# Performance work log

Hardware: AMD Instinct MI355X
Metric: run time of the kernel (lower is better)

Reference implementation:

```python
import jax, jax.numpy as jnp
import numpy as np

HM_W, WH_W, OFF_W = 1.0, 0.1, 1.0  # loss_weight dict values
EPS_SIG = 1e-4


def _neg_loss(pred, gt):
    # pred already sigmoided + clamped. Modified focal loss (CornerNet).
    pos = (gt == 1.0).astype(pred.dtype)
    neg = (gt < 1.0).astype(pred.dtype)
    part1 = (pos + (2.0 * neg - 1.0) * pred) ** 2          # alpha=2
    part2 = (neg + (2.0 * pos - 1.0) * gt) ** 4            # beta=4
    part3 = jnp.log(neg + (2.0 * pos - 1.0) * pred)
    loss = -jnp.sum(part1 * part2 * part3)
    num_pos = jnp.sum(pos)
    fallback = jnp.maximum(jnp.sum((pred > 0.3).astype(pred.dtype)), 1.0)
    denom = jnp.where(num_pos == 0.0, fallback, num_pos)
    return loss / denom


def _reg_l1(pred, mask, ind, target):
    # pred: [B,C,H,W] -> gather K per-object C-dim vectors per batch via flat HW index
    B, C, H, W = pred.shape
    K = ind.shape[1]
    feat = pred.transpose(0, 2, 3, 1).reshape(B, H * W, C)  # [B,HW,C]
    idx = jnp.broadcast_to(ind[:, :, None], (B, K, C))
    gathered = jnp.take_along_axis(feat, idx, axis=1)       # [B,K,C]
    m = jnp.broadcast_to(mask[:, :, None].astype(pred.dtype), (B, K, C))
    diff = gathered * m - target * m
    ad = jnp.abs(diff)
    sl1 = jnp.where(ad < 1.0, 0.5 * diff * diff, ad - 0.5)  # smooth_l1, sum
    return jnp.sum(sl1) / (jnp.sum(m) + 1e-4)


def setup_inputs() -> dict:
    key = jax.random.key(0)
    ks = jax.random.split(key, 8)
    B, C, H, W, K = 128, 20, 128, 128, 128
    hm_pred = jax.random.normal(ks[0], (B, C, H, W), dtype=jnp.float32)
    hm_gt = jax.random.uniform(ks[1], (B, C, H, W), dtype=jnp.float32)
    # plant some exact positives (gt == 1) like real CenterNet targets
    hm_gt = hm_gt.at[:, :, 64, 64].set(1.0)
    wh_pred = jax.random.normal(ks[2], (B, 2, H, W), dtype=jnp.float32)
    wh_gt = jax.random.uniform(ks[3], (B, K, 2), dtype=jnp.float32)
    off_pred = jax.random.normal(ks[4], (B, 2, H, W), dtype=jnp.float32)
    off_gt = jax.random.uniform(ks[5], (B, K, 2), dtype=jnp.float32)
    offset_mask = jax.random.randint(ks[6], (B, K), 0, 2, dtype=jnp.int32)
    indexes = jax.random.randint(ks[7], (B, K), 0, H * W).astype(jnp.int64)
    return {"hm_pred": hm_pred, "hm_gt": hm_gt, "wh_pred": wh_pred,
            "wh_gt": wh_gt, "off_pred": off_pred, "off_gt": off_gt,
            "offset_mask": offset_mask, "indexes": indexes}


def reference(hm_pred, hm_gt, wh_pred, wh_gt, off_pred, off_gt, offset_mask, indexes):
    hm = jnp.clip(jax.nn.sigmoid(hm_pred), EPS_SIG, 1.0 - EPS_SIG)
    hm_loss = _neg_loss(hm, hm_gt)
    wh_loss = _reg_l1(wh_pred, offset_mask, indexes, wh_gt)
    off_loss = _reg_l1(off_pred, offset_mask, indexes, off_gt)
    total = HM_W * hm_loss + WH_W * wh_loss + OFF_W * off_loss
    return (hm_loss, wh_loss, off_loss, total)
```

## Files before the change

### kernel.cpp

```cpp
#include <hip/hip_runtime.h>

#define NB_HM   2048
#define NB_REG  64
#define REG_OFF (3 * NB_HM)

typedef float f32x4 __attribute__((ext_vector_type(4)));

__device__ __forceinline__ float wave_sum(float v) {
    #pragma unroll
    for (int off = 32; off > 0; off >>= 1) v += __shfl_down(v, off, 64);
    return v;
}

__device__ __forceinline__ void block_reduce_store3(float a, float b, float c,
                                                    float* __restrict__ dst) {
    a = wave_sum(a); b = wave_sum(b); c = wave_sum(c);
    __shared__ float sa[8], sb[8], sc[8];
    int lane = threadIdx.x & 63;
    int wave = threadIdx.x >> 6;
    if (lane == 0) { sa[wave] = a; sb[wave] = b; sc[wave] = c; }
    __syncthreads();
    if (threadIdx.x == 0) {
        int nw = blockDim.x >> 6;
        float ta = 0.f, tb = 0.f, tc = 0.f;
        for (int w = 0; w < nw; ++w) { ta += sa[w]; tb += sb[w]; tc += sc[w]; }
        dst[0] = ta; dst[1] = tb; dst[2] = tc;
    }
}

__device__ __forceinline__ void hm_elem(float x, float gt, float& s_loss,
                                        unsigned& posc, unsigned& cntc) {
    bool pos = (gt == 1.0f);
    float e = __expf(-x);
    float p = __builtin_amdgcn_rcpf(1.0f + e);
    p = fminf(fmaxf(p, 1e-4f), 1.0f - 1e-4f);
    float arg = pos ? p : 1.0f - p;
    float a   = 1.0f - arg;
    float b   = pos ? 1.0f : 1.0f - gt;
    float b2  = b * b;
    float l   = __logf(arg);
    s_loss += (a * a) * (b2 * b2) * l;
    posc += (unsigned)__popcll(__ballot(pos));
    cntc += (unsigned)__popcll(__ballot(p > 0.3f));
}

__device__ __forceinline__ void gload(f32x4& d, const f32x4* a) {
    asm volatile("global_load_dwordx4 %0, %1, off" : "=v"(d) : "v"(a));
}

#define SB() __builtin_amdgcn_sched_barrier(0)
#define WAITV(n) do { asm volatile("s_waitcnt vmcnt(" #n ")" ::: "memory"); SB(); } while (0)

#define COMPV(P, G)                                    \
    do {                                               \
        hm_elem((P)[0], (G)[0], s_loss, posc, cntc);   \
        hm_elem((P)[1], (G)[1], s_loss, posc, cntc);   \
        hm_elem((P)[2], (G)[2], s_loss, posc, cntc);   \
        hm_elem((P)[3], (G)[3], s_loss, posc, cntc);   \
    } while (0)

#define PH_MID(SET, CNEXT)                                        \
    do {                                                          \
        WAITV(6);                                                 \
        COMPV(P##SET, G##SET);                                    \
        SB();                                                     \
        const f32x4* _pa = pp + (long long)(CNEXT) * NT;          \
        const f32x4* _ga = gg + (long long)(CNEXT) * NT;          \
        gload(P##SET, _pa);                                       \
        gload(G##SET, _ga);                                       \
    } while (0)

#define PH_TAIL(SET, WN)                                          \
    do { WAITV(WN); COMPV(P##SET, G##SET); SB(); } while (0)

__global__ void __launch_bounds__(256)
hm_loss_kernel(const f32x4* __restrict__ p4,
               const f32x4* __restrict__ g4,
               float* __restrict__ ws, long long N4) {
    long long tid = (long long)blockIdx.x * blockDim.x + threadIdx.x;
    long long NT  = (long long)gridDim.x * blockDim.x;

    float    s_loss = 0.f;
    unsigned posc = 0, cntc = 0;

    bool clean = (N4 == 20 * NT);

    if (clean) {
        f32x4 P0, P1, P2, P3, G0, G1, G2, G3;
        const f32x4* pp = p4 + tid;
        const f32x4* gg = g4 + tid;

        gload(P0, pp);              gload(G0, gg);
        gload(P1, pp + NT);         gload(G1, gg + NT);
        gload(P2, pp + 2 * NT);     gload(G2, gg + 2 * NT);
        gload(P3, pp + 3 * NT);     gload(G3, gg + 3 * NT);

        PH_MID(0, 4);   PH_MID(1, 5);   PH_MID(2, 6);   PH_MID(3, 7);
        PH_MID(0, 8);   PH_MID(1, 9);   PH_MID(2, 10);  PH_MID(3, 11);
        PH_MID(0, 12);  PH_MID(1, 13);  PH_MID(2, 14);  PH_MID(3, 15);
        PH_MID(0, 16);  PH_MID(1, 17);  PH_MID(2, 18);  PH_MID(3, 19);

        PH_TAIL(0, 6);  PH_TAIL(1, 4);  PH_TAIL(2, 2);  PH_TAIL(3, 0);
    } else {
        for (long long i = tid; i < N4; i += NT) {
            f32x4 xp = p4[i];
            f32x4 xg = g4[i];
            COMPV(xp, xg);
        }
    }

    int lane = threadIdx.x & 63;
    float fpos = (lane == 0) ? (float)posc : 0.f;
    float fcnt = (lane == 0) ? (float)cntc : 0.f;
    block_reduce_store3(s_loss, fpos, fcnt, &ws[3 * (size_t)blockIdx.x]);
}

__device__ __forceinline__ float smooth_l1(float d) {
    float ad = fabsf(d);
    return (ad < 1.0f) ? 0.5f * d * d : ad - 0.5f;
}

__global__ void __launch_bounds__(256)
reg_loss_kernel(const float* __restrict__ wh_pred,  const float* __restrict__ wh_gt,
                const float* __restrict__ off_pred, const float* __restrict__ off_gt,
                const int* __restrict__ mask, const int* __restrict__ ind,
                float* __restrict__ ws, int BK, int K, int HW) {
    int t = blockIdx.x * blockDim.x + threadIdx.x;
    int nt = gridDim.x * blockDim.x;
    float s_wh = 0.f, s_off = 0.f, s_m = 0.f;

    for (int i = t; i < BK; i += nt) {
        int b   = i / K;
        float m = (float)mask[i];
        int idx = ind[i];
        const float* wb = wh_pred  + (size_t)b * 2 * HW;
        const float* ob = off_pred + (size_t)b * 2 * HW;
        #pragma unroll
        for (int c = 0; c < 2; ++c) {
            float gw = wb[(size_t)c * HW + idx];
            float tw = wh_gt[(size_t)i * 2 + c];
            s_wh += smooth_l1(gw * m - tw * m);

            float go = ob[(size_t)c * HW + idx];
            float to = off_gt[(size_t)i * 2 + c];
            s_off += smooth_l1(go * m - to * m);
        }
        s_m += 2.0f * m;
    }

    block_reduce_store3(s_wh, s_off, s_m, &ws[REG_OFF + 3 * (size_t)blockIdx.x]);
}

__global__ void __launch_bounds__(1024)
reduce_finalize_kernel(const float* __restrict__ ws, float* __restrict__ out) {
    float a = 0.f, b = 0.f, c = 0.f, w = 0.f, o = 0.f, m = 0.f;
    for (int i = threadIdx.x; i < NB_HM; i += 1024) {
        a += ws[3 * i + 0];
        b += ws[3 * i + 1];
        c += ws[3 * i + 2];
    }
    if (threadIdx.x < 3 * NB_REG) {
        float v = ws[REG_OFF + threadIdx.x];
        int r = threadIdx.x % 3;
        w = (r == 0) ? v : 0.f;
        o = (r == 1) ? v : 0.f;
        m = (r == 2) ? v : 0.f;
    }

    a = wave_sum(a); b = wave_sum(b); c = wave_sum(c);
    w = wave_sum(w); o = wave_sum(o); m = wave_sum(m);

    __shared__ float s[6][16];
    int lane = threadIdx.x & 63, wv = threadIdx.x >> 6;
    if (lane == 0) {
        s[0][wv] = a; s[1][wv] = b; s[2][wv] = c;
        s[3][wv] = w; s[4][wv] = o; s[5][wv] = m;
    }
    __syncthreads();
    if (threadIdx.x == 0) {
        float t[6];
        #pragma unroll
        for (int k = 0; k < 6; ++k) {
            float acc = 0.f;
            for (int q = 0; q < 16; ++q) acc += s[k][q];
            t[k] = acc;
        }
        float loss_sum = -t[0];
        float num_pos  = t[1];
        float fallback = fmaxf(t[2], 1.0f);
        float denom    = (num_pos == 0.0f) ? fallback : num_pos;
        float hm_loss  = loss_sum / denom;
        float md       = t[5] + 1e-4f;
        float wh_loss  = t[3] / md;
        float off_loss = t[4] / md;
        out[0] = hm_loss;
        out[1] = wh_loss;
        out[2] = off_loss;
        out[3] = hm_loss + 0.1f * wh_loss + off_loss;
    }
}

extern "C" void kernel_launch(void* const* d_in, const int* in_sizes, int n_in,
                              void* d_out, int out_size, void* d_ws, size_t ws_size,
                              hipStream_t stream) {
    const float* hm_pred  = (const float*)d_in[0];
    const float* hm_gt    = (const float*)d_in[1];
    const float* wh_pred  = (const float*)d_in[2];
    const float* wh_gt    = (const float*)d_in[3];
    const float* off_pred = (const float*)d_in[4];
    const float* off_gt   = (const float*)d_in[5];
    const int*   mask     = (const int*)d_in[6];
    const int*   ind      = (const int*)d_in[7];
    float*       out      = (float*)d_out;
    float*       ws       = (float*)d_ws;

    long long N  = in_sizes[0];
    int       BK = in_sizes[6];
    const int K  = 128;
    int       B  = BK / K;
    int       HW = in_sizes[2] / (2 * B);

    hm_loss_kernel<<<NB_HM, 256, 0, stream>>>((const f32x4*)hm_pred,
                                              (const f32x4*)hm_gt, ws, N >> 2);
    reg_loss_kernel<<<NB_REG, 256, 0, stream>>>(wh_pred, wh_gt, off_pred, off_gt,
                                                mask, ind, ws, BK, K, HW);
    reduce_finalize_kernel<<<1, 1024, 0, stream>>>(ws, out);
}
```

Before: 80.44 us.

## Fuse heatmap, regression and finalize into one kernel with last-block reduction

Merges the three kernel launches into one grid where the first blocks compute the heatmap focal loss and a few extra blocks compute the gathered regression losses. An atomic counter elects the last finishing block to run the final reduction, so the separate finalize launch goes away. A memset resets the counter before each launch. The hand-scheduled inline-asm load pipeline is replaced by a plain 4-way unrolled loop, which hands load scheduling back to the compiler and may lose some memory-level overlap.

```diff
diff --git a/kernel.cpp b/kernel.cpp
--- a/kernel.cpp
+++ b/kernel.cpp
@@ -1,8 +1,10 @@
 #include <hip/hip_runtime.h>
 
 #define NB_HM   2048
-#define NB_REG  64
+#define NB_REG  8
+#define NBLK    (NB_HM + NB_REG)
 #define REG_OFF (3 * NB_HM)
+#define CTR_IDX 8192
 
 typedef float f32x4 __attribute__((ext_vector_type(4)));
 
@@ -15,15 +17,15 @@
 __device__ __forceinline__ void block_reduce_store3(float a, float b, float c,
                                                     float* __restrict__ dst) {
     a = wave_sum(a); b = wave_sum(b); c = wave_sum(c);
-    __shared__ float sa[8], sb[8], sc[8];
+    __shared__ float sa[4], sb[4], sc[4];
     int lane = threadIdx.x & 63;
     int wave = threadIdx.x >> 6;
     if (lane == 0) { sa[wave] = a; sb[wave] = b; sc[wave] = c; }
     __syncthreads();
     if (threadIdx.x == 0) {
-        int nw = blockDim.x >> 6;
         float ta = 0.f, tb = 0.f, tc = 0.f;
-        for (int w = 0; w < nw; ++w) { ta += sa[w]; tb += sb[w]; tc += sc[w]; }
+        #pragma unroll
+        for (int w = 0; w < 4; ++w) { ta += sa[w]; tb += sb[w]; tc += sc[w]; }
         dst[0] = ta; dst[1] = tb; dst[2] = tc;
     }
 }
@@ -44,13 +46,6 @@
     cntc += (unsigned)__popcll(__ballot(p > 0.3f));
 }
 
-__device__ __forceinline__ void gload(f32x4& d, const f32x4* a) {
-    asm volatile("global_load_dwordx4 %0, %1, off" : "=v"(d) : "v"(a));
-}
-
-#define SB() __builtin_amdgcn_sched_barrier(0)
-#define WAITV(n) do { asm volatile("s_waitcnt vmcnt(" #n ")" ::: "memory"); SB(); } while (0)
-
 #define COMPV(P, G)                                    \
     do {                                               \
         hm_elem((P)[0], (G)[0], s_loss, posc, cntc);   \
@@ -59,144 +54,132 @@
         hm_elem((P)[3], (G)[3], s_loss, posc, cntc);   \
     } while (0)
 
-#define PH_MID(SET, CNEXT)                                        \
-    do {                                                          \
-        WAITV(6);                                                 \
-        COMPV(P##SET, G##SET);                                    \
-        SB();                                                     \
-        const f32x4* _pa = pp + (long long)(CNEXT) * NT;          \
-        const f32x4* _ga = gg + (long long)(CNEXT) * NT;          \
-        gload(P##SET, _pa);                                       \
-        gload(G##SET, _ga);                                       \
-    } while (0)
-
-#define PH_TAIL(SET, WN)                                          \
-    do { WAITV(WN); COMPV(P##SET, G##SET); SB(); } while (0)
+__device__ __forceinline__ float smooth_l1(float d) {
+    float ad = fabsf(d);
+    return (ad < 1.0f) ? 0.5f * d * d : ad - 0.5f;
+}
 
 __global__ void __launch_bounds__(256)
-hm_loss_kernel(const f32x4* __restrict__ p4,
-               const f32x4* __restrict__ g4,
-               float* __restrict__ ws, long long N4) {
-    long long tid = (long long)blockIdx.x * blockDim.x + threadIdx.x;
-    long long NT  = (long long)gridDim.x * blockDim.x;
-
-    float    s_loss = 0.f;
-    unsigned posc = 0, cntc = 0;
-
-    bool clean = (N4 == 20 * NT);
-
-    if (clean) {
-        f32x4 P0, P1, P2, P3, G0, G1, G2, G3;
-        const f32x4* pp = p4 + tid;
-        const f32x4* gg = g4 + tid;
-
-        gload(P0, pp);              gload(G0, gg);
-        gload(P1, pp + NT);         gload(G1, gg + NT);
-        gload(P2, pp + 2 * NT);     gload(G2, gg + 2 * NT);
-        gload(P3, pp + 3 * NT);     gload(G3, gg + 3 * NT);
-
-        PH_MID(0, 4);   PH_MID(1, 5);   PH_MID(2, 6);   PH_MID(3, 7);
-        PH_MID(0, 8);   PH_MID(1, 9);   PH_MID(2, 10);  PH_MID(3, 11);
-        PH_MID(0, 12);  PH_MID(1, 13);  PH_MID(2, 14);  PH_MID(3, 15);
-        PH_MID(0, 16);  PH_MID(1, 17);  PH_MID(2, 18);  PH_MID(3, 19);
-
-        PH_TAIL(0, 6);  PH_TAIL(1, 4);  PH_TAIL(2, 2);  PH_TAIL(3, 0);
-    } else {
-        for (long long i = tid; i < N4; i += NT) {
+fused_loss_kernel(const f32x4* __restrict__ p4, const f32x4* __restrict__ g4,
+                  long long N4,
+                  const float* __restrict__ wh_pred,  const float* __restrict__ wh_gt,
+                  const float* __restrict__ off_pred, const float* __restrict__ off_gt,
+                  const int* __restrict__ mask, const int* __restrict__ ind,
+                  int BK, int K, int HW,
+                  float* __restrict__ ws, float* __restrict__ out) {
+    if (blockIdx.x < NB_HM) {
+        long long tid = (long long)blockIdx.x * 256 + threadIdx.x;
+        long long NT  = (long long)NB_HM * 256;
+
+        float    s_loss = 0.f;
+        unsigned posc = 0, cntc = 0;
+
+        long long i = tid;
+        for (; i + 3 * NT < N4; i += 4 * NT) {
+            f32x4 xp0 = p4[i];
+            f32x4 xp1 = p4[i + NT];
+            f32x4 xp2 = p4[i + 2 * NT];
+            f32x4 xp3 = p4[i + 3 * NT];
+            f32x4 xg0 = g4[i];
+            f32x4 xg1 = g4[i + NT];
+            f32x4 xg2 = g4[i + 2 * NT];
+            f32x4 xg3 = g4[i + 3 * NT];
+            COMPV(xp0, xg0);
+            COMPV(xp1, xg1);
+            COMPV(xp2, xg2);
+            COMPV(xp3, xg3);
+        }
+        for (; i < N4; i += NT) {
             f32x4 xp = p4[i];
             f32x4 xg = g4[i];
             COMPV(xp, xg);
         }
-    }
-
-    int lane = threadIdx.x & 63;
-    float fpos = (lane == 0) ? (float)posc : 0.f;
-    float fcnt = (lane == 0) ? (float)cntc : 0.f;
-    block_reduce_store3(s_loss, fpos, fcnt, &ws[3 * (size_t)blockIdx.x]);
-}
-
-__device__ __forceinline__ float smooth_l1(float d) {
-    float ad = fabsf(d);
-    return (ad < 1.0f) ? 0.5f * d * d : ad - 0.5f;
-}
-
-__global__ void __launch_bounds__(256)
-reg_loss_kernel(const float* __restrict__ wh_pred,  const float* __restrict__ wh_gt,
-                const float* __restrict__ off_pred, const float* __restrict__ off_gt,
-                const int* __restrict__ mask, const int* __restrict__ ind,
-                float* __restrict__ ws, int BK, int K, int HW) {
-    int t = blockIdx.x * blockDim.x + threadIdx.x;
-    int nt = gridDim.x * blockDim.x;
-    float s_wh = 0.f, s_off = 0.f, s_m = 0.f;
-
-    for (int i = t; i < BK; i += nt) {
-        int b   = i / K;
-        float m = (float)mask[i];
-        int idx = ind[i];
-        const float* wb = wh_pred  + (size_t)b * 2 * HW;
-        const float* ob = off_pred + (size_t)b * 2 * HW;
-        #pragma unroll
-        for (int c = 0; c < 2; ++c) {
-            float gw = wb[(size_t)c * HW + idx];
-            float tw = wh_gt[(size_t)i * 2 + c];
-            s_wh += smooth_l1(gw * m - tw * m);
-
-            float go = ob[(size_t)c * HW + idx];
-            float to = off_gt[(size_t)i * 2 + c];
-            s_off += smooth_l1(go * m - to * m);
-        }
-        s_m += 2.0f * m;
-    }
-
-    block_reduce_store3(s_wh, s_off, s_m, &ws[REG_OFF + 3 * (size_t)blockIdx.x]);
-}
-
-__global__ void __launch_bounds__(1024)
-reduce_finalize_kernel(const float* __restrict__ ws, float* __restrict__ out) {
-    float a = 0.f, b = 0.f, c = 0.f, w = 0.f, o = 0.f, m = 0.f;
-    for (int i = threadIdx.x; i < NB_HM; i += 1024) {
-        a += ws[3 * i + 0];
-        b += ws[3 * i + 1];
-        c += ws[3 * i + 2];
-    }
-    if (threadIdx.x < 3 * NB_REG) {
-        float v = ws[REG_OFF + threadIdx.x];
-        int r = threadIdx.x % 3;
-        w = (r == 0) ? v : 0.f;
-        o = (r == 1) ? v : 0.f;
-        m = (r == 2) ? v : 0.f;
-    }
-
-    a = wave_sum(a); b = wave_sum(b); c = wave_sum(c);
-    w = wave_sum(w); o = wave_sum(o); m = wave_sum(m);
-
-    __shared__ float s[6][16];
-    int lane = threadIdx.x & 63, wv = threadIdx.x >> 6;
-    if (lane == 0) {
-        s[0][wv] = a; s[1][wv] = b; s[2][wv] = c;
-        s[3][wv] = w; s[4][wv] = o; s[5][wv] = m;
+
+        int lane = threadIdx.x & 63;
+        float fpos = (lane == 0) ? (float)posc : 0.f;
+        float fcnt = (lane == 0) ? (float)cntc : 0.f;
+        block_reduce_store3(s_loss, fpos, fcnt, &ws[3 * (size_t)blockIdx.x]);
+    } else {
+        int t  = (blockIdx.x - NB_HM) * 256 + threadIdx.x;
+        int nt = NB_REG * 256;
+        float s_wh = 0.f, s_off = 0.f, s_m = 0.f;
+
+        for (int i = t; i < BK; i += nt) {
+            int b   = i / K;
+            float m = (float)mask[i];
+            int idx = ind[i];
+            const float* wb = wh_pred  + (size_t)b * 2 * HW;
+            const float* ob = off_pred + (size_t)b * 2 * HW;
+            #pragma unroll
+            for (int c = 0; c < 2; ++c) {
+                float gw = wb[(size_t)c * HW + idx];
+                float tw = wh_gt[(size_t)i * 2 + c];
+                s_wh += smooth_l1(gw * m - tw * m);
+
+                float go = ob[(size_t)c * HW + idx];
+                float to = off_gt[(size_t)i * 2 + c];
+                s_off += smooth_l1(go * m - to * m);
+            }
+            s_m += 2.0f * m;
+        }
+
+        block_reduce_store3(s_wh, s_off, s_m,
+                            &ws[REG_OFF + 3 * (size_t)(blockIdx.x - NB_HM)]);
+    }
+
+    __shared__ int s_last;
+    if (threadIdx.x == 0) {
+        __threadfence();
+        int* ctr = (int*)&ws[CTR_IDX];
+        int old = atomicAdd(ctr, 1);
+        s_last = (old == NBLK - 1) ? 1 : 0;
     }
     __syncthreads();
-    if (threadIdx.x == 0) {
-        float t[6];
-        #pragma unroll
-        for (int k = 0; k < 6; ++k) {
-            float acc = 0.f;
-            for (int q = 0; q < 16; ++q) acc += s[k][q];
-            t[k] = acc;
-        }
-        float loss_sum = -t[0];
-        float num_pos  = t[1];
-        float fallback = fmaxf(t[2], 1.0f);
-        float denom    = (num_pos == 0.0f) ? fallback : num_pos;
-        float hm_loss  = loss_sum / denom;
-        float md       = t[5] + 1e-4f;
-        float wh_loss  = t[3] / md;
-        float off_loss = t[4] / md;
-        out[0] = hm_loss;
-        out[1] = wh_loss;
-        out[2] = off_loss;
-        out[3] = hm_loss + 0.1f * wh_loss + off_loss;
+    if (s_last) {
+        __threadfence();
+        float a = 0.f, b = 0.f, c = 0.f, w = 0.f, o = 0.f, m = 0.f;
+        for (int i = threadIdx.x; i < NB_HM; i += 256) {
+            a += ws[3 * i + 0];
+            b += ws[3 * i + 1];
+            c += ws[3 * i + 2];
+        }
+        if (threadIdx.x < 3 * NB_REG) {
+            float v = ws[REG_OFF + threadIdx.x];
+            int r = threadIdx.x % 3;
+            w = (r == 0) ? v : 0.f;
+            o = (r == 1) ? v : 0.f;
+            m = (r == 2) ? v : 0.f;
+        }
+
+        a = wave_sum(a); b = wave_sum(b); c = wave_sum(c);
+        w = wave_sum(w); o = wave_sum(o); m = wave_sum(m);
+
+        __shared__ float s[6][4];
+        int lane = threadIdx.x & 63, wv = threadIdx.x >> 6;
+        if (lane == 0) {
+            s[0][wv] = a; s[1][wv] = b; s[2][wv] = c;
+            s[3][wv] = w; s[4][wv] = o; s[5][wv] = m;
+        }
+        __syncthreads();
+        if (threadIdx.x == 0) {
+            float t[6];
+            #pragma unroll
+            for (int k = 0; k < 6; ++k)
+                t[k] = s[k][0] + s[k][1] + s[k][2] + s[k][3];
+
+            float loss_sum = -t[0];
+            float num_pos  = t[1];
+            float fallback = fmaxf(t[2], 1.0f);
+            float denom    = (num_pos == 0.0f) ? fallback : num_pos;
+            float hm_loss  = loss_sum / denom;
+            float md       = t[5] + 1e-4f;
+            float wh_loss  = t[3] / md;
+            float off_loss = t[4] / md;
+            out[0] = hm_loss;
+            out[1] = wh_loss;
+            out[2] = off_loss;
+            out[3] = hm_loss + 0.1f * wh_loss + off_loss;
+        }
     }
 }
 
@@ -220,9 +203,10 @@
     int       B  = BK / K;
     int       HW = in_sizes[2] / (2 * B);
 
-    hm_loss_kernel<<<NB_HM, 256, 0, stream>>>((const f32x4*)hm_pred,
-                                              (const f32x4*)hm_gt, ws, N >> 2);
-    reg_loss_kernel<<<NB_REG, 256, 0, stream>>>(wh_pred, wh_gt, off_pred, off_gt,
-                                                mask, ind, ws, BK, K, HW);
-    reduce_finalize_kernel<<<1, 1024, 0, stream>>>(ws, out);
-}
+    hipMemsetAsync((char*)d_ws + CTR_IDX * sizeof(float), 0, sizeof(int), stream);
+
+    fused_loss_kernel<<<NBLK, 256, 0, stream>>>(
+        (const f32x4*)hm_pred, (const f32x4*)hm_gt, N >> 2,
+        wh_pred, wh_gt, off_pred, off_gt, mask, ind, BK, K, HW,
+        ws, out);
+}
```

New measurement: 182.9 us. +127.4%, slower.

## Replace grid-stride asm pipeline with contiguous per-block chunks and compiler loads

Applied to the files above, without the earlier changes.

The heatmap kernel drops its hand-scheduled inline-asm load pipeline, which read grid-strided chunks. Each block now handles one contiguous chunk of the input, using plain loads unrolled four at a time, with a remainder loop. The aim is better DRAM page and cache locality per block and letting the compiler schedule loads. The cost is giving up the explicit deep software prefetch, so each group of four loads is now waited on before compute with no overlap into the next group.

```diff
diff --git a/kernel.cpp b/kernel.cpp
--- a/kernel.cpp
+++ b/kernel.cpp
@@ -44,13 +44,6 @@
     cntc += (unsigned)__popcll(__ballot(p > 0.3f));
 }
 
-__device__ __forceinline__ void gload(f32x4& d, const f32x4* a) {
-    asm volatile("global_load_dwordx4 %0, %1, off" : "=v"(d) : "v"(a));
-}
-
-#define SB() __builtin_amdgcn_sched_barrier(0)
-#define WAITV(n) do { asm volatile("s_waitcnt vmcnt(" #n ")" ::: "memory"); SB(); } while (0)
-
 #define COMPV(P, G)                                    \
     do {                                               \
         hm_elem((P)[0], (G)[0], s_loss, posc, cntc);   \
@@ -59,49 +52,41 @@
         hm_elem((P)[3], (G)[3], s_loss, posc, cntc);   \
     } while (0)
 
-#define PH_MID(SET, CNEXT)                                        \
-    do {                                                          \
-        WAITV(6);                                                 \
-        COMPV(P##SET, G##SET);                                    \
-        SB();                                                     \
-        const f32x4* _pa = pp + (long long)(CNEXT) * NT;          \
-        const f32x4* _ga = gg + (long long)(CNEXT) * NT;          \
-        gload(P##SET, _pa);                                       \
-        gload(G##SET, _ga);                                       \
-    } while (0)
-
-#define PH_TAIL(SET, WN)                                          \
-    do { WAITV(WN); COMPV(P##SET, G##SET); SB(); } while (0)
-
 __global__ void __launch_bounds__(256)
 hm_loss_kernel(const f32x4* __restrict__ p4,
                const f32x4* __restrict__ g4,
                float* __restrict__ ws, long long N4) {
-    long long tid = (long long)blockIdx.x * blockDim.x + threadIdx.x;
-    long long NT  = (long long)gridDim.x * blockDim.x;
-
     float    s_loss = 0.f;
     unsigned posc = 0, cntc = 0;
 
-    bool clean = (N4 == 20 * NT);
-
-    if (clean) {
-        f32x4 P0, P1, P2, P3, G0, G1, G2, G3;
-        const f32x4* pp = p4 + tid;
-        const f32x4* gg = g4 + tid;
-
-        gload(P0, pp);              gload(G0, gg);
-        gload(P1, pp + NT);         gload(G1, gg + NT);
-        gload(P2, pp + 2 * NT);     gload(G2, gg + 2 * NT);
-        gload(P3, pp + 3 * NT);     gload(G3, gg + 3 * NT);
-
-        PH_MID(0, 4);   PH_MID(1, 5);   PH_MID(2, 6);   PH_MID(3, 7);
-        PH_MID(0, 8);   PH_MID(1, 9);   PH_MID(2, 10);  PH_MID(3, 11);
-        PH_MID(0, 12);  PH_MID(1, 13);  PH_MID(2, 14);  PH_MID(3, 15);
-        PH_MID(0, 16);  PH_MID(1, 17);  PH_MID(2, 18);  PH_MID(3, 19);
-
-        PH_TAIL(0, 6);  PH_TAIL(1, 4);  PH_TAIL(2, 2);  PH_TAIL(3, 0);
+    if ((N4 % ((long long)NB_HM * 256)) == 0) {
+        long long per_block = N4 / NB_HM;
+        long long nIter     = per_block >> 8;
+        long long i = (long long)blockIdx.x * per_block + threadIdx.x;
+
+        long long j = 0;
+        for (; j + 3 < nIter; j += 4, i += 1024) {
+            f32x4 xp0 = p4[i];
+            f32x4 xp1 = p4[i + 256];
+            f32x4 xp2 = p4[i + 512];
+            f32x4 xp3 = p4[i + 768];
+            f32x4 xg0 = g4[i];
+            f32x4 xg1 = g4[i + 256];
+            f32x4 xg2 = g4[i + 512];
+            f32x4 xg3 = g4[i + 768];
+            COMPV(xp0, xg0);
+            COMPV(xp1, xg1);
+            COMPV(xp2, xg2);
+            COMPV(xp3, xg3);
+        }
+        for (; j < nIter; ++j, i += 256) {
+            f32x4 xp = p4[i];
+            f32x4 xg = g4[i];
+            COMPV(xp, xg);
+        }
     } else {
+        long long tid = (long long)blockIdx.x * blockDim.x + threadIdx.x;
+        long long NT  = (long long)gridDim.x * blockDim.x;
         for (long long i = tid; i < N4; i += NT) {
             f32x4 xp = p4[i];
             f32x4 xg = g4[i];
```

New measurement: 72.14 us (median of 2 runs). 10.3% less time.
